# Performance work log

Measured on AMD Instinct MI355X. Metric: run time of the kernel, lower is better.

## Reference

```python
import jax, jax.numpy as jnp
import numpy as np

B = 32          # graphs in batch
NP = 1000       # nodes per graph (uniform -> static TopK)
N = B * NP      # total nodes
DEG = 10
E = N * DEG     # intra-graph edges
H, D = 4, 128   # heads, per-head dim (GATConv(32,128,heads=4))
F_IN = 32
HD = H * D      # 512
K = int(np.ceil(0.8 * NP))  # TopKPooling ratio=0.8 -> 800 kept per graph
SLOPE = 0.2     # GATConv leaky_relu negative slope


def setup_inputs() -> dict:
    key = jax.random.key(0)
    ks = jax.random.split(key, 16)
    x = jax.random.normal(ks[0], (N, F_IN), jnp.float32)
    off = (jnp.arange(B, dtype=jnp.int64) * NP)[:, None]
    src = (jax.random.randint(ks[1], (B, NP * DEG), 0, NP) + off).reshape(-1)
    dst = (jax.random.randint(ks[2], (B, NP * DEG), 0, NP) + off).reshape(-1)
    edge_index = jnp.stack([src, dst]).astype(jnp.int64)
    batch = jnp.repeat(jnp.arange(B, dtype=jnp.int64), NP)
    edge_attr = jax.random.normal(ks[3], (E, 16), jnp.float32)
    # GATConv params
    W = jax.random.normal(ks[4], (F_IN, HD), jnp.float32) / np.sqrt(F_IN)
    att_src = jax.random.normal(ks[5], (H, D), jnp.float32) * 0.1
    att_dst = jax.random.normal(ks[6], (H, D), jnp.float32) * 0.1
    bias = jnp.zeros((HD,), jnp.float32)
    # TopKPooling weight
    topk_w = jax.random.normal(ks[7], (HD,), jnp.float32)
    # MLP head
    lin1_w = jax.random.normal(ks[8], (2 * HD, 128), jnp.float32) / np.sqrt(2 * HD)
    lin1_b = jnp.zeros((128,), jnp.float32)
    lin2_w = jax.random.normal(ks[9], (128, 64), jnp.float32) / np.sqrt(128)
    lin2_b = jnp.zeros((64,), jnp.float32)
    lin3_w = jax.random.normal(ks[10], (64, 8), jnp.float32) / np.sqrt(64)
    lin3_b = jnp.zeros((8,), jnp.float32)
    return dict(x=x, edge_index=edge_index, batch=batch, edge_attr=edge_attr,
                W=W, att_src=att_src, att_dst=att_dst, bias=bias, topk_w=topk_w,
                lin1_w=lin1_w, lin1_b=lin1_b, lin2_w=lin2_w, lin2_b=lin2_b,
                lin3_w=lin3_w, lin3_b=lin3_b)


def reference(x, edge_index, batch, edge_attr, W, att_src, att_dst, bias, topk_w,
              lin1_w, lin1_b, lin2_w, lin2_b, lin3_w, lin3_b):
    # ---- GATConv(32,128,heads=4), concat, default self-loops ----
    loop = jnp.arange(N, dtype=edge_index.dtype)
    src = jnp.concatenate([edge_index[0], loop])
    dst = jnp.concatenate([edge_index[1], loop])
    h = (x @ W).reshape(N, H, D)                       # [N,H,D]
    a_s = jnp.einsum('nhd,hd->nh', h, att_src)         # [N,H]
    a_d = jnp.einsum('nhd,hd->nh', h, att_dst)
    e = jax.nn.leaky_relu(a_s[src] + a_d[dst], SLOPE)  # [E2,H]
    m = jax.ops.segment_max(e, dst, num_segments=N)    # per-dst softmax (stable)
    ex = jnp.exp(e - m[dst])
    denom = jax.ops.segment_sum(ex, dst, num_segments=N)
    alpha = ex / denom[dst]                            # [E2,H]
    agg = jax.ops.segment_sum(alpha[:, :, None] * h[src], dst, num_segments=N)
    x1 = jax.nn.relu(agg.reshape(N, HD) + bias)        # [N,512]
    # ---- TopKPooling(512, ratio=0.8), tanh nonlinearity ----
    score = jnp.tanh((x1 @ topk_w) / jnp.linalg.norm(topk_w))  # [N]
    vals, idx = jax.lax.top_k(score.reshape(B, NP), K)         # [B,K]
    xg = x1.reshape(B, NP, HD)
    xs = jnp.take_along_axis(xg, idx[:, :, None], axis=1) * vals[:, :, None]
    # ---- global max + mean pool, MLP head (eval: dropout = identity) ----
    x2 = jnp.concatenate([xs.max(axis=1), xs.mean(axis=1)], axis=-1)  # [B,1024]
    h1 = jax.nn.relu(x2 @ lin1_w + lin1_b)
    h2 = jax.nn.relu(h1 @ lin2_w + lin2_b)
    return jax.nn.log_softmax(h2 @ lin3_w + lin3_b, axis=-1)  # [B,8]
```

## Files before the change

### kernel.cpp

```cpp
#include <hip/hip_runtime.h>
#include <hip/hip_fp16.h>
#include <math.h>


#define N_NODES 32000
#define B_GRAPHS 32
#define NPG 1000
#define DEGC 10
#define E_EDGES (N_NODES*DEGC)
#define HD 512
#define F_IN 32
#define KKEEP 800
#define SLOPE 0.2f
#define CAP 32

__global__ void prep_kernel(const float* __restrict__ W, const float* __restrict__ att_src,
                            const float* __restrict__ att_dst, const float* __restrict__ topk_w,
                            float* __restrict__ Ws, float* __restrict__ Wd, float* __restrict__ misc,
                            int* __restrict__ counts)
{
    int tid = threadIdx.x;
    if (blockIdx.x > 0) {
        int i = (blockIdx.x - 1)*256 + tid;
        if (i < N_NODES/4) ((int4*)counts)[i] = make_int4(0,0,0,0);
        return;
    }
    if (tid < 128) {
        int f = tid >> 2, hh = tid & 3;
        float s1 = 0.f, s2 = 0.f;
        for (int d = 0; d < 128; ++d) {
            float w = W[f*HD + hh*128 + d];
            s1 = fmaf(w, att_src[hh*128 + d], s1);
            s2 = fmaf(w, att_dst[hh*128 + d], s2);
        }
        Ws[f*4+hh] = s1;
        Wd[f*4+hh] = s2;
    }
    __shared__ float red[256];
    float tw0 = topk_w[tid], tw1 = topk_w[tid+256];
    red[tid] = tw0*tw0 + tw1*tw1;
    __syncthreads();
    for (int s = 128; s > 0; s >>= 1) { if (tid < s) red[tid] += red[tid+s]; __syncthreads(); }
    if (tid == 0) misc[0] = 1.0f / sqrtf(red[0]);
}

#define NPB 32
#define CH_BLOCKS 1000
#define BS_BLOCKS 128
__global__ __launch_bounds__(256) void stage1_kernel(
    const float* __restrict__ x, const float* __restrict__ W,
    const float* __restrict__ Ws, const float* __restrict__ Wd,
    const int* __restrict__ dst,
    __half* __restrict__ h, float* __restrict__ a_s, float* __restrict__ a_d,
    int* __restrict__ counts, int* __restrict__ slots)
{
    int b = blockIdx.x;
    int tid = threadIdx.x;
    if (b < CH_BLOCKS) {
        __shared__ float s_x[NPB*F_IN];
        int n0 = (b & 7)*4000 + (b >> 3)*NPB;
        float wc0[F_IN], wc1[F_IN];
        #pragma unroll
        for (int f = 0; f < F_IN; ++f) {
            float2 wp = *(const float2*)(W + f*HD + 2*tid);
            wc0[f] = wp.x;
            wc1[f] = wp.y;
        }
        const float4* xg = (const float4*)(x + (size_t)n0*F_IN);
        float4* sx4 = (float4*)s_x;
        if (tid < NPB*F_IN/4) sx4[tid] = xg[tid];
        __syncthreads();
        for (int n = 0; n < NPB; ++n) {
            const float4* xr = (const float4*)(s_x + n*F_IN);
            float acc0 = 0.f, acc1 = 0.f;
            #pragma unroll
            for (int f4 = 0; f4 < F_IN/4; ++f4) {
                float4 xv = xr[f4];
                acc0 = fmaf(xv.x, wc0[f4*4+0], acc0); acc1 = fmaf(xv.x, wc1[f4*4+0], acc1);
                acc0 = fmaf(xv.y, wc0[f4*4+1], acc0); acc1 = fmaf(xv.y, wc1[f4*4+1], acc1);
                acc0 = fmaf(xv.z, wc0[f4*4+2], acc0); acc1 = fmaf(xv.z, wc1[f4*4+2], acc1);
                acc0 = fmaf(xv.w, wc0[f4*4+3], acc0); acc1 = fmaf(xv.w, wc1[f4*4+3], acc1);
            }
            *(__half2*)(h + (size_t)(n0+n)*HD + 2*tid) = __floats2half2_rn(acc0, acc1);
        }
        {
            int n = tid >> 3, hh = (tid >> 1) & 3, which = tid & 1;
            const float* Wx = which ? Wd : Ws;
            const float* xr = s_x + n*F_IN;
            float s = 0.f;
            #pragma unroll
            for (int f = 0; f < F_IN; ++f) s = fmaf(xr[f], Wx[f*4+hh], s);
            float* dp = which ? a_d : a_s;
            dp[(size_t)(n0+n)*4 + hh] = s;
        }
    } else {
        int i = (b - CH_BLOCKS)*256 + tid;
        int stride = BS_BLOCKS*256;
        for (; i < E_EDGES; i += stride) {
            int d = dst[i];
            int p = atomicAdd(&counts[d], 1);
            if (p < CAP) slots[d*CAP + p] = i;
        }
    }
}

__global__ __launch_bounds__(256) void gat_agg_kernel(
    const __half* __restrict__ h, const float* __restrict__ a_s, const float* __restrict__ a_d,
    const int* __restrict__ counts, const int* __restrict__ slots, const int* __restrict__ esrc,
    const float* __restrict__ bias, const float* __restrict__ topk_w, const float* __restrict__ misc,
    __half* __restrict__ x1, float* __restrict__ scores)
{
    __shared__ int    s_src[4][CAP];
    __shared__ float4 s_al4[4][CAP];
    int tid = threadIdx.x;
    int wid = tid >> 6, lane = tid & 63;
    int grp  = (blockIdx.x & 7) * 1000 + (blockIdx.x >> 3);
    int node = grp*4 + wid;
    int deg  = min(counts[node], CAP);

    int src = node;
    if (lane < deg) src = esrc[slots[node*CAP + lane]];

    float4 ad    = *(const float4*)(a_d + (size_t)node*4);
    float4 aself = *(const float4*)(a_s + (size_t)node*4);
    float4 asrc  = make_float4(0.f,0.f,0.f,0.f);
    if (lane < deg) asrc = *(const float4*)(a_s + (size_t)src*4);

    float ex[4], exs[4];
    {
        float u;
        u = asrc.x + ad.x;  ex[0]  = u > 0.f ? u : SLOPE*u;
        u = asrc.y + ad.y;  ex[1]  = u > 0.f ? u : SLOPE*u;
        u = asrc.z + ad.z;  ex[2]  = u > 0.f ? u : SLOPE*u;
        u = asrc.w + ad.w;  ex[3]  = u > 0.f ? u : SLOPE*u;
        u = aself.x + ad.x; exs[0] = __expf(u > 0.f ? u : SLOPE*u);
        u = aself.y + ad.y; exs[1] = __expf(u > 0.f ? u : SLOPE*u);
        u = aself.z + ad.z; exs[2] = __expf(u > 0.f ? u : SLOPE*u);
        u = aself.w + ad.w; exs[3] = __expf(u > 0.f ? u : SLOPE*u);
    }
    float al[4], alself[4];
    #pragma unroll
    for (int hh = 0; hh < 4; ++hh) {
        float e = (lane < deg) ? __expf(ex[hh]) : 0.f;
        float den = e;
        #pragma unroll
        for (int msk = 1; msk < 64; msk <<= 1) den += __shfl_xor(den, msk, 64);
        den += exs[hh];
        float inv = __builtin_amdgcn_rcpf(den);
        al[hh]     = e * inv;
        alself[hh] = exs[hh] * inv;
    }
    if (lane < deg) {
        s_src[wid][lane] = src;
        s_al4[wid][lane] = make_float4(al[0], al[1], al[2], al[3]);
    }
    __syncthreads();

    int head = lane >> 4;
    const __half* hb = h + lane*8;
    const float* alw = (const float*)&s_al4[wid][0];
    float f0=0.f,f1=0.f,f2=0.f,f3=0.f,f4=0.f,f5=0.f,f6=0.f,f7=0.f;
    #define MIX_LO(ACC,A,Q) asm("v_fma_mix_f32 %0, %1, %2, %0 op_sel_hi:[0,1,0]" : "+v"(ACC) : "v"(A), "v"(Q))
    #define MIX_HI(ACC,A,Q) asm("v_fma_mix_f32 %0, %1, %2, %0 op_sel:[0,1,0] op_sel_hi:[0,1,0]" : "+v"(ACC) : "v"(A), "v"(Q))
    #define MIX8(AV,Q) { \
        MIX_LO(f0, AV, Q.x); MIX_HI(f1, AV, Q.x); \
        MIX_LO(f2, AV, Q.y); MIX_HI(f3, AV, Q.y); \
        MIX_LO(f4, AV, Q.z); MIX_HI(f5, AV, Q.z); \
        MIX_LO(f6, AV, Q.w); MIX_HI(f7, AV, Q.w); }
    int e = 0;
    for (; e + 4 <= deg; e += 4) {
        int se0 = s_src[wid][e],   se1 = s_src[wid][e+1];
        int se2 = s_src[wid][e+2], se3 = s_src[wid][e+3];
        float av0 = alw[(e+0)*4 + head], av1 = alw[(e+1)*4 + head];
        float av2 = alw[(e+2)*4 + head], av3 = alw[(e+3)*4 + head];
        uint4 q0 = *(const uint4*)(hb + (size_t)se0*HD);
        uint4 q1 = *(const uint4*)(hb + (size_t)se1*HD);
        uint4 q2 = *(const uint4*)(hb + (size_t)se2*HD);
        uint4 q3 = *(const uint4*)(hb + (size_t)se3*HD);
        MIX8(av0, q0) MIX8(av1, q1) MIX8(av2, q2) MIX8(av3, q3)
    }
    for (; e < deg; ++e) {
        int se = s_src[wid][e];
        float av = alw[e*4 + head];
        uint4 q = *(const uint4*)(hb + (size_t)se*HD);
        MIX8(av, q)
    }
    {
        float a01 = (head & 1) ? alself[1] : alself[0];
        float a23 = (head & 1) ? alself[3] : alself[2];
        float av  = (head & 2) ? a23 : a01;
        uint4 q = *(const uint4*)(hb + (size_t)node*HD);
        MIX8(av, q)
    }
    #undef MIX8
    #undef MIX_LO
    #undef MIX_HI

    int c0 = lane*8;
    float4 b0 = *(const float4*)(bias + c0);
    float4 b1 = *(const float4*)(bias + c0 + 4);
    float v0 = fmaxf(f0 + b0.x, 0.f), v1 = fmaxf(f1 + b0.y, 0.f);
    float v2 = fmaxf(f2 + b0.z, 0.f), v3 = fmaxf(f3 + b0.w, 0.f);
    float v4 = fmaxf(f4 + b1.x, 0.f), v5 = fmaxf(f5 + b1.y, 0.f);
    float v6 = fmaxf(f6 + b1.z, 0.f), v7 = fmaxf(f7 + b1.w, 0.f);
    {
        __half2 p0 = __floats2half2_rn(v0, v1);
        __half2 p1 = __floats2half2_rn(v2, v3);
        __half2 p2 = __floats2half2_rn(v4, v5);
        __half2 p3 = __floats2half2_rn(v6, v7);
        uint4 pk;
        pk.x = *(unsigned*)&p0; pk.y = *(unsigned*)&p1;
        pk.z = *(unsigned*)&p2; pk.w = *(unsigned*)&p3;
        *(uint4*)(x1 + (size_t)node*HD + c0) = pk;
    }

    float4 tw0 = *(const float4*)(topk_w + c0);
    float4 tw1 = *(const float4*)(topk_w + c0 + 4);
    float p = v0*tw0.x + v1*tw0.y + v2*tw0.z + v3*tw0.w
            + v4*tw1.x + v5*tw1.y + v6*tw1.z + v7*tw1.w;
    #pragma unroll
    for (int msk = 1; msk < 64; msk <<= 1) p += __shfl_xor(p, msk, 64);
    if (lane == 0) {
        float dotv = p * misc[0];
        float eu   = __expf(2.f * fabsf(dotv));
        float th   = 1.f - 2.f/(eu + 1.f);
        scores[node] = copysignf(th, dotv);
    }
}

__global__ __launch_bounds__(256) void topk_kernel(const float* __restrict__ scores,
                                                   int* __restrict__ kept_ids,
                                                   float* __restrict__ kept_vals)
{
    int g = blockIdx.x, part = blockIdx.y;
    __shared__ float s[NPG];
    int tid = threadIdx.x;
    for (int i = tid; i < NPG; i += 256) s[i] = scores[g*NPG + i];
    __syncthreads();
    int i = part*250 + tid;
    if (tid < 250) {
        float si = s[i];
        int rank = 0;
        for (int j = 0; j < NPG; ++j) {
            float sj = s[j];
            rank += (sj > si) || (sj == si && j < i);
        }
        if (rank < KKEEP) {
            kept_ids[g*KKEEP + rank]  = g*NPG + i;
            kept_vals[g*KKEEP + rank] = si;
        }
    }
}

#define RCHUNK 50
#define NCHUNK 16
__global__ __launch_bounds__(128) void pool_partial_kernel(
    const __half* __restrict__ x1, const int* __restrict__ kept_ids,
    const float* __restrict__ kept_vals, float* __restrict__ pmax, float* __restrict__ psum)
{
    int bid = blockIdx.x;
    int k = bid & 7, q = bid >> 3;
    int g = k*4 + (q & 3), c = q >> 2;
    int tid = threadIdx.x;
    __shared__ int   ids[RCHUNK];
    __shared__ float vals[RCHUNK];
    if (tid < RCHUNK) {
        ids[tid]  = kept_ids[g*KKEEP + c*RCHUNK + tid];
        vals[tid] = kept_vals[g*KKEEP + c*RCHUNK + tid];
    }
    __syncthreads();
    float4 mxA = make_float4(-INFINITY,-INFINITY,-INFINITY,-INFINITY), mxB = mxA;
    float4 smA = make_float4(0.f,0.f,0.f,0.f), smB = smA;
    for (int r = 0; r < RCHUNK; r += 2) {
        const __half2* pA = (const __half2*)(x1 + (size_t)ids[r]*HD + tid*4);
        const __half2* pB = (const __half2*)(x1 + (size_t)ids[r+1]*HD + tid*4);
        __half2 qA0 = pA[0], qA1 = pA[1], qB0 = pB[0], qB1 = pB[1];
        float2 a0 = __half22float2(qA0), a1 = __half22float2(qA1);
        float2 b0 = __half22float2(qB0), b1 = __half22float2(qB1);
        float lA = vals[r], lB = vals[r+1];
        float4 vA = make_float4(a0.x*lA, a0.y*lA, a1.x*lA, a1.y*lA);
        float4 vB = make_float4(b0.x*lB, b0.y*lB, b1.x*lB, b1.y*lB);
        mxA.x = fmaxf(mxA.x, vA.x); mxA.y = fmaxf(mxA.y, vA.y);
        mxA.z = fmaxf(mxA.z, vA.z); mxA.w = fmaxf(mxA.w, vA.w);
        mxB.x = fmaxf(mxB.x, vB.x); mxB.y = fmaxf(mxB.y, vB.y);
        mxB.z = fmaxf(mxB.z, vB.z); mxB.w = fmaxf(mxB.w, vB.w);
        smA.x += vA.x; smA.y += vA.y; smA.z += vA.z; smA.w += vA.w;
        smB.x += vB.x; smB.y += vB.y; smB.z += vB.z; smB.w += vB.w;
    }
    float4 mx, sm;
    mx.x = fmaxf(mxA.x, mxB.x); mx.y = fmaxf(mxA.y, mxB.y);
    mx.z = fmaxf(mxA.z, mxB.z); mx.w = fmaxf(mxA.w, mxB.w);
    sm.x = smA.x + smB.x; sm.y = smA.y + smB.y;
    sm.z = smA.z + smB.z; sm.w = smA.w + smB.w;
    *(float4*)(pmax + (size_t)(g*NCHUNK + c)*HD + tid*4) = mx;
    *(float4*)(psum + (size_t)(g*NCHUNK + c)*HD + tid*4) = sm;
}

__global__ __launch_bounds__(256) void mlp_kernel(
    const float* __restrict__ pmax, const float* __restrict__ psum,
    const float* __restrict__ w1, const float* __restrict__ b1,
    const float* __restrict__ w2, const float* __restrict__ b2,
    const float* __restrict__ w3, const float* __restrict__ b3,
    float* __restrict__ out)
{
    int g = blockIdx.x;
    int tid = threadIdx.x;
    __shared__ float sx[1024];
    __shared__ float part1[8][128];
    __shared__ float sh1[128];
    __shared__ float part2[4][64];
    __shared__ float sh2[64];
    __shared__ float part3[8][8];
    __shared__ float slog[8];

    {
        int half = tid >> 7;
        int c4 = tid & 127;
        const float* basep = half ? psum : pmax;
        float4 r = *(const float4*)(basep + (size_t)(g*NCHUNK)*HD + c4*4);
        #pragma unroll
        for (int c = 1; c < NCHUNK; ++c) {
            float4 v = *(const float4*)(basep + (size_t)(g*NCHUNK + c)*HD + c4*4);
            if (half) { r.x += v.x; r.y += v.y; r.z += v.z; r.w += v.w; }
            else {
                r.x = fmaxf(r.x, v.x); r.y = fmaxf(r.y, v.y);
                r.z = fmaxf(r.z, v.z); r.w = fmaxf(r.w, v.w);
            }
        }
        if (half) { const float inv = 1.0f/KKEEP; r.x *= inv; r.y *= inv; r.z *= inv; r.w *= inv; }
        *(float4*)(sx + half*512 + c4*4) = r;
    }
    __syncthreads();

    {
        int ks = tid >> 5, tc = tid & 31;
        const float* w1p = w1 + (size_t)(ks*128)*128 + tc*4;
        const float* sxp = sx + ks*128;
        float4 acc = make_float4(0.f,0.f,0.f,0.f);
        #pragma unroll 8
        for (int k = 0; k < 128; ++k) {
            float xk = sxp[k];
            float4 w = *(const float4*)(w1p + (size_t)k*128);
            acc.x = fmaf(xk, w.x, acc.x); acc.y = fmaf(xk, w.y, acc.y);
            acc.z = fmaf(xk, w.z, acc.z); acc.w = fmaf(xk, w.w, acc.w);
        }
        *(float4*)(&part1[ks][tc*4]) = acc;
    }
    __syncthreads();
    if (tid < 128) {
        float s = b1[tid];
        #pragma unroll
        for (int p = 0; p < 8; ++p) s += part1[p][tid];
        sh1[tid] = fmaxf(s, 0.0f);
    }
    __syncthreads();

    {
        int ks2 = tid >> 6, to = tid & 63;
        float a = 0.f;
        #pragma unroll 8
        for (int k = 0; k < 32; ++k) {
            int kk = ks2*32 + k;
            a = fmaf(sh1[kk], w2[kk*64 + to], a);
        }
        part2[ks2][to] = a;
    }
    __syncthreads();
    if (tid < 64) {
        float s = b2[tid];
        #pragma unroll
        for (int p = 0; p < 4; ++p) s += part2[p][tid];
        sh2[tid] = fmaxf(s, 0.0f);
    }
    __syncthreads();

    if (tid < 64) {
        int ks3 = tid >> 3, o = tid & 7;
        float a = 0.f;
        #pragma unroll
        for (int k = 0; k < 8; ++k) {
            int kk = ks3*8 + k;
            a = fmaf(sh2[kk], w3[kk*8 + o], a);
        }
        part3[ks3][o] = a;
    }
    __syncthreads();
    if (tid < 8) {
        float s = b3[tid];
        #pragma unroll
        for (int p = 0; p < 8; ++p) s += part3[p][tid];
        slog[tid] = s;
    }
    __syncthreads();
    if (tid == 0) {
        float m = slog[0];
        for (int i = 1; i < 8; ++i) m = fmaxf(m, slog[i]);
        float ssum = 0.0f;
        for (int i = 0; i < 8; ++i) ssum += expf(slog[i] - m);
        float lse = m + logf(ssum);
        for (int i = 0; i < 8; ++i) out[g*8 + i] = slog[i] - lse;
    }
}

extern "C" void kernel_launch(void* const* d_in, const int* in_sizes, int n_in,
                              void* d_out, int out_size, void* d_ws, size_t ws_size,
                              hipStream_t stream) {
    const float* x        = (const float*)d_in[0];
    const int*   ei       = (const int*)d_in[1];
    const float* W        = (const float*)d_in[4];
    const float* att_src  = (const float*)d_in[5];
    const float* att_dst  = (const float*)d_in[6];
    const float* bias     = (const float*)d_in[7];
    const float* topk_w   = (const float*)d_in[8];
    const float* w1       = (const float*)d_in[9];
    const float* b1       = (const float*)d_in[10];
    const float* w2       = (const float*)d_in[11];
    const float* b2       = (const float*)d_in[12];
    const float* w3       = (const float*)d_in[13];
    const float* b3       = (const float*)d_in[14];
    float* out = (float*)d_out;

    const int* src = ei;
    const int* dst = ei + E_EDGES;

    char* wsb = (char*)d_ws;
    size_t off = 0;
    auto alloc = [&](size_t bytes) -> void* {
        void* p = (void*)(wsb + off);
        off += (bytes + 255) & ~(size_t)255;
        return p;
    };
    __half* h       = (__half*)alloc((size_t)N_NODES*HD*2);
    __half* x1      = (__half*)alloc((size_t)N_NODES*HD*2);
    float* a_s      = (float*)alloc((size_t)N_NODES*4*4);
    float* a_d      = (float*)alloc((size_t)N_NODES*4*4);
    float* Ws       = (float*)alloc(F_IN*4*4);
    float* Wd       = (float*)alloc(F_IN*4*4);
    float* misc     = (float*)alloc(256);
    int*   counts   = (int*)alloc((size_t)N_NODES*4);
    int*   slots    = (int*)alloc((size_t)N_NODES*CAP*4);
    float* scores   = (float*)alloc((size_t)N_NODES*4);
    int*   kept_ids = (int*)alloc((size_t)B_GRAPHS*KKEEP*4);
    float* kept_vals= (float*)alloc((size_t)B_GRAPHS*KKEEP*4);
    float* pmax     = (float*)alloc((size_t)B_GRAPHS*NCHUNK*HD*4);
    float* psum     = (float*)alloc((size_t)B_GRAPHS*NCHUNK*HD*4);

    prep_kernel<<<33, 256, 0, stream>>>(W, att_src, att_dst, topk_w, Ws, Wd, misc, counts);
    stage1_kernel<<<CH_BLOCKS + BS_BLOCKS, 256, 0, stream>>>(
        x, W, Ws, Wd, dst, h, a_s, a_d, counts, slots);
    gat_agg_kernel<<<N_NODES/4, 256, 0, stream>>>(h, a_s, a_d, counts, slots, src,
                                                  bias, topk_w, misc, x1, scores);
    topk_kernel<<<dim3(B_GRAPHS, 4), 256, 0, stream>>>(scores, kept_ids, kept_vals);
    pool_partial_kernel<<<B_GRAPHS*NCHUNK, 128, 0, stream>>>(x1, kept_ids, kept_vals, pmax, psum);
    mlp_kernel<<<B_GRAPHS, 256, 0, stream>>>(pmax, psum, w1, b1, w2, b2, w3, b3, out);
}
```

Before: 117.5 us.

## Fuse MLP head into pooling kernel via last-block-done atomic counter

Merges the pooling-partial and MLP kernels. Each pooling block writes its partial max/sum, fences, and bumps a per-graph atomic counter, and the last block for each graph reduces the partials and runs the MLP with 128 threads. A zeroed counter array is added to prep_kernel. This removes one kernel launch and its gap, in exchange for fence/atomic overhead and an MLP tail run at half the previous thread count.

Result: slower. 142.2 us (+21.1%).

```diff
diff --git a/kernel.cpp b/kernel.cpp
--- a/kernel.cpp
+++ b/kernel.cpp
@@ -17,7 +17,7 @@
 __global__ void prep_kernel(const float* __restrict__ W, const float* __restrict__ att_src,
                             const float* __restrict__ att_dst, const float* __restrict__ topk_w,
                             float* __restrict__ Ws, float* __restrict__ Wd, float* __restrict__ misc,
-                            int* __restrict__ counts)
+                            int* __restrict__ counts, int* __restrict__ done)
 {
     int tid = threadIdx.x;
     if (blockIdx.x > 0) {
@@ -25,6 +25,7 @@
         if (i < N_NODES/4) ((int4*)counts)[i] = make_int4(0,0,0,0);
         return;
     }
+    if (tid < B_GRAPHS) done[tid] = 0;
     if (tid < 128) {
         int f = tid >> 2, hh = tid & 3;
         float s1 = 0.f, s2 = 0.f;
@@ -254,9 +255,14 @@
 
 #define RCHUNK 50
 #define NCHUNK 16
-__global__ __launch_bounds__(128) void pool_partial_kernel(
+__global__ __launch_bounds__(128) void pool_mlp_kernel(
     const __half* __restrict__ x1, const int* __restrict__ kept_ids,
-    const float* __restrict__ kept_vals, float* __restrict__ pmax, float* __restrict__ psum)
+    const float* __restrict__ kept_vals, float* __restrict__ pmax, float* __restrict__ psum,
+    int* __restrict__ done,
+    const float* __restrict__ w1, const float* __restrict__ b1,
+    const float* __restrict__ w2, const float* __restrict__ b2,
+    const float* __restrict__ w3, const float* __restrict__ b3,
+    float* __restrict__ out)
 {
     int bid = blockIdx.x;
     int k = bid & 7, q = bid >> 3;
@@ -294,63 +300,59 @@
     sm.z = smA.z + smB.z; sm.w = smA.w + smB.w;
     *(float4*)(pmax + (size_t)(g*NCHUNK + c)*HD + tid*4) = mx;
     *(float4*)(psum + (size_t)(g*NCHUNK + c)*HD + tid*4) = sm;
-}
-
-__global__ __launch_bounds__(256) void mlp_kernel(
-    const float* __restrict__ pmax, const float* __restrict__ psum,
-    const float* __restrict__ w1, const float* __restrict__ b1,
-    const float* __restrict__ w2, const float* __restrict__ b2,
-    const float* __restrict__ w3, const float* __restrict__ b3,
-    float* __restrict__ out)
-{
-    int g = blockIdx.x;
-    int tid = threadIdx.x;
+
+    __threadfence();
+    __shared__ int amlast;
+    if (tid == 0) amlast = (atomicAdd(&done[g], 1) == NCHUNK - 1);
+    __syncthreads();
+    if (!amlast) return;
+    __threadfence();
+
     __shared__ float sx[1024];
-    __shared__ float part1[8][128];
+    __shared__ float part1[4][128];
     __shared__ float sh1[128];
-    __shared__ float part2[4][64];
+    __shared__ float part2[2][64];
     __shared__ float sh2[64];
     __shared__ float part3[8][8];
     __shared__ float slog[8];
 
     {
-        int half = tid >> 7;
-        int c4 = tid & 127;
-        const float* basep = half ? psum : pmax;
-        float4 r = *(const float4*)(basep + (size_t)(g*NCHUNK)*HD + c4*4);
-        #pragma unroll
-        for (int c = 1; c < NCHUNK; ++c) {
-            float4 v = *(const float4*)(basep + (size_t)(g*NCHUNK + c)*HD + c4*4);
-            if (half) { r.x += v.x; r.y += v.y; r.z += v.z; r.w += v.w; }
-            else {
-                r.x = fmaxf(r.x, v.x); r.y = fmaxf(r.y, v.y);
-                r.z = fmaxf(r.z, v.z); r.w = fmaxf(r.w, v.w);
-            }
-        }
-        if (half) { const float inv = 1.0f/KKEEP; r.x *= inv; r.y *= inv; r.z *= inv; r.w *= inv; }
-        *(float4*)(sx + half*512 + c4*4) = r;
+        float4 rm = *(const float4*)(pmax + (size_t)(g*NCHUNK)*HD + tid*4);
+        float4 rs = *(const float4*)(psum + (size_t)(g*NCHUNK)*HD + tid*4);
+        #pragma unroll
+        for (int cc = 1; cc < NCHUNK; ++cc) {
+            float4 vm = *(const float4*)(pmax + (size_t)(g*NCHUNK + cc)*HD + tid*4);
+            float4 vs = *(const float4*)(psum + (size_t)(g*NCHUNK + cc)*HD + tid*4);
+            rm.x = fmaxf(rm.x, vm.x); rm.y = fmaxf(rm.y, vm.y);
+            rm.z = fmaxf(rm.z, vm.z); rm.w = fmaxf(rm.w, vm.w);
+            rs.x += vs.x; rs.y += vs.y; rs.z += vs.z; rs.w += vs.w;
+        }
+        const float inv = 1.0f/KKEEP;
+        rs.x *= inv; rs.y *= inv; rs.z *= inv; rs.w *= inv;
+        *(float4*)(sx + tid*4)       = rm;
+        *(float4*)(sx + 512 + tid*4) = rs;
     }
     __syncthreads();
 
     {
         int ks = tid >> 5, tc = tid & 31;
-        const float* w1p = w1 + (size_t)(ks*128)*128 + tc*4;
-        const float* sxp = sx + ks*128;
+        const float* w1p = w1 + (size_t)(ks*256)*128 + tc*4;
+        const float* sxp = sx + ks*256;
         float4 acc = make_float4(0.f,0.f,0.f,0.f);
         #pragma unroll 8
-        for (int k = 0; k < 128; ++k) {
-            float xk = sxp[k];
-            float4 w = *(const float4*)(w1p + (size_t)k*128);
+        for (int kk = 0; kk < 256; ++kk) {
+            float xk = sxp[kk];
+            float4 w = *(const float4*)(w1p + (size_t)kk*128);
             acc.x = fmaf(xk, w.x, acc.x); acc.y = fmaf(xk, w.y, acc.y);
             acc.z = fmaf(xk, w.z, acc.z); acc.w = fmaf(xk, w.w, acc.w);
         }
         *(float4*)(&part1[ks][tc*4]) = acc;
     }
     __syncthreads();
-    if (tid < 128) {
+    {
         float s = b1[tid];
         #pragma unroll
-        for (int p = 0; p < 8; ++p) s += part1[p][tid];
+        for (int p = 0; p < 4; ++p) s += part1[p][tid];
         sh1[tid] = fmaxf(s, 0.0f);
     }
     __syncthreads();
@@ -359,17 +361,16 @@
         int ks2 = tid >> 6, to = tid & 63;
         float a = 0.f;
         #pragma unroll 8
-        for (int k = 0; k < 32; ++k) {
-            int kk = ks2*32 + k;
-            a = fmaf(sh1[kk], w2[kk*64 + to], a);
+        for (int kk = 0; kk < 64; ++kk) {
+            int kx = ks2*64 + kk;
+            a = fmaf(sh1[kx], w2[kx*64 + to], a);
         }
         part2[ks2][to] = a;
     }
     __syncthreads();
     if (tid < 64) {
         float s = b2[tid];
-        #pragma unroll
-        for (int p = 0; p < 4; ++p) s += part2[p][tid];
+        s += part2[0][tid] + part2[1][tid];
         sh2[tid] = fmaxf(s, 0.0f);
     }
     __syncthreads();
@@ -378,9 +379,9 @@
         int ks3 = tid >> 3, o = tid & 7;
         float a = 0.f;
         #pragma unroll
-        for (int k = 0; k < 8; ++k) {
-            int kk = ks3*8 + k;
-            a = fmaf(sh2[kk], w3[kk*8 + o], a);
+        for (int kk = 0; kk < 8; ++kk) {
+            int kx = ks3*8 + kk;
+            a = fmaf(sh2[kx], w3[kx*8 + o], a);
         }
         part3[ks3][o] = a;
     }
@@ -444,13 +445,14 @@
     float* kept_vals= (float*)alloc((size_t)B_GRAPHS*KKEEP*4);
     float* pmax     = (float*)alloc((size_t)B_GRAPHS*NCHUNK*HD*4);
     float* psum     = (float*)alloc((size_t)B_GRAPHS*NCHUNK*HD*4);
-
-    prep_kernel<<<33, 256, 0, stream>>>(W, att_src, att_dst, topk_w, Ws, Wd, misc, counts);
+    int*   done     = (int*)alloc((size_t)B_GRAPHS*4);
+
+    prep_kernel<<<33, 256, 0, stream>>>(W, att_src, att_dst, topk_w, Ws, Wd, misc, counts, done);
     stage1_kernel<<<CH_BLOCKS + BS_BLOCKS, 256, 0, stream>>>(
         x, W, Ws, Wd, dst, h, a_s, a_d, counts, slots);
     gat_agg_kernel<<<N_NODES/4, 256, 0, stream>>>(h, a_s, a_d, counts, slots, src,
                                                   bias, topk_w, misc, x1, scores);
     topk_kernel<<<dim3(B_GRAPHS, 4), 256, 0, stream>>>(scores, kept_ids, kept_vals);
-    pool_partial_kernel<<<B_GRAPHS*NCHUNK, 128, 0, stream>>>(x1, kept_ids, kept_vals, pmax, psum);
-    mlp_kernel<<<B_GRAPHS, 256, 0, stream>>>(pmax, psum, w1, b1, w2, b2, w3, b3, out);
-}
+    pool_mlp_kernel<<<B_GRAPHS*NCHUNK, 128, 0, stream>>>(x1, kept_ids, kept_vals, pmax, psum,
+                                                         done, w1, b1, w2, b2, w3, b3, out);
+}
```
